# Kernel optimization log

Measured on AMD Instinct MI355X. Metric: run time of the kernel, lower is better.

The kernel has to match this reference:

```python
import jax, jax.numpy as jnp
import numpy as np

L, H, C, V, B, T, Q = 6, 8, 512, 32000, 2, 4096, 256
N = C // H
LN_EPS = 1e-5
GN_EPS = 1e-5 * 64  # matches nn.GroupNorm(n_head, C, eps=1e-05*64)


def _shift(x):
    # ZeroPad2d((0,0,1,-1)): x[t] -> x[t-1], zero at t=0
    return jnp.concatenate([jnp.zeros_like(x[:, :1]), x[:, :-1]], axis=1)


def _layernorm(x, w):
    mu = x.mean(-1, keepdims=True)
    var = jnp.var(x, axis=-1, keepdims=True)
    return (x - mu) * jax.lax.rsqrt(var + LN_EPS) * w


def _time_mix(x, maa_k, maa_v, maa_r, maa_g, tdecay, tfaaaa, Wr, Wk, Wv, Wg, Wo, gn_w, gn_b):
    Bsz, Tlen, Cd = x.shape
    xx = _shift(x) - x
    xk = x + xx * maa_k
    xv = x + xx * maa_v
    xr = x + xx * maa_r
    xg = x + xx * maa_g
    r = (xr @ Wr.T).reshape(Bsz, Tlen, H, N).transpose(0, 2, 1, 3)   # B H T N
    k = (xk @ Wk.T).reshape(Bsz, Tlen, H, N).transpose(0, 2, 3, 1)   # B H N T
    v = (xv @ Wv.T).reshape(Bsz, Tlen, H, N).transpose(0, 2, 1, 3)   # B H T N
    g = jax.nn.silu(xg @ Wg.T)
    wdec = jnp.exp(-jnp.exp(tdecay))            # [H], per-head decay in (0,1)
    u = tfaaaa                                  # [H], 'first token' bonus
    ws = (wdec ** Q)[None, :, None, None]       # state decay across a chunk
    jj = jnp.arange(Q)
    wkv = (wdec[:, None] ** (Q - 1 - jj))[None, :, None, :]  # [1,H,1,Q]
    wb = (wdec[:, None] ** jj)[None, :, :, None]              # [1,H,Q,1]
    d = jj[:, None] - jj[None, :]                              # i - j
    # intra-chunk decay matrix: W[i,j] = u (i==j), wdec^(i-j-1) (i>j), 0 (i<j)
    Wmat = jnp.where(d > 0, wdec[:, None, None] ** jnp.maximum(d - 1, 0), 0.0)
    Wmat = (Wmat + u[:, None, None] * jnp.eye(Q, dtype=x.dtype))[None]  # [1,H,Q,Q]
    nc = Tlen // Q
    rc = r.reshape(Bsz, H, nc, Q, N).transpose(2, 0, 1, 3, 4)  # [nc,B,H,Q,N]
    kc = k.reshape(Bsz, H, N, nc, Q).transpose(3, 0, 1, 2, 4)  # [nc,B,H,N,Q]
    vc = v.reshape(Bsz, H, nc, Q, N).transpose(2, 0, 1, 3, 4)  # [nc,B,H,Q,N]

    def step(state, inp):
        rr, kk, vv = inp
        y = ((rr @ kk) * Wmat) @ vv + (rr @ state) * wb
        new_state = ws * state + (kk * wkv) @ vv
        return new_state, y

    state0 = jnp.zeros((Bsz, H, N, N), dtype=x.dtype)
    _, yc = jax.lax.scan(step, state0, (rc, kc, vc))
    y = yc.transpose(1, 2, 0, 3, 4).reshape(Bsz, H, Tlen, N).transpose(0, 2, 1, 3)  # B T H N
    # GroupNorm(n_head groups) == per (b,t,h) normalization over head dim N
    mu = y.mean(-1, keepdims=True)
    var = jnp.var(y, axis=-1, keepdims=True)
    y = (y - mu) * jax.lax.rsqrt(var + GN_EPS)
    y = y.reshape(Bsz, Tlen, Cd) * gn_w + gn_b
    return (y * g) @ Wo.T


def _channel_mix(x, cmaa_k, cmaa_r, Wck, Wcv, Wcr):
    xx = _shift(x) - x
    xk = x + xx * cmaa_k
    xr = x + xx * cmaa_r
    h = jnp.square(jax.nn.relu(xk @ Wck.T))
    h = h @ Wcv.T
    return jax.nn.sigmoid(xr @ Wcr.T) * h


def _forward(idx, wte, wpe, ln1_w, ln2_w, lnf_w, maa_k, maa_v, maa_r, maa_g, tdecay, tfaaaa,
             Wr, Wk, Wv, Wg, Wo, gn_w, gn_b, cmaa_k, cmaa_r, Wck, Wcv, Wcr):
    t = idx.shape[1]
    x = wte[idx] + wpe[:t]
    for l in range(L):
        x = x + _time_mix(_layernorm(x, ln1_w[l]), maa_k[l], maa_v[l], maa_r[l], maa_g[l],
                          tdecay[l], tfaaaa[l], Wr[l], Wk[l], Wv[l], Wg[l], Wo[l], gn_w[l], gn_b[l])
        x = x + _channel_mix(_layernorm(x, ln2_w[l]), cmaa_k[l], cmaa_r[l], Wck[l], Wcv[l], Wcr[l])
    x = _layernorm(x, lnf_w)
    logits = x[:, -1:, :] @ wte.T  # targets=None path: only last position
    return logits


def setup_inputs() -> dict:
    key = jax.random.key(0)
    ks = jax.random.split(key, 12)
    idx = jax.random.randint(ks[0], (B, T), 0, V)
    # structured per-layer init tensors (exact formulas from __init__)
    ddd = np.arange(C, dtype=np.float32) / C
    hh = np.arange(H, dtype=np.float32) / (H - 1)
    maa_k = np.zeros((L, C), np.float32); maa_v = np.zeros((L, C), np.float32)
    maa_r = np.zeros((L, C), np.float32); maa_g = np.zeros((L, C), np.float32)
    tdecay = np.zeros((L, H), np.float32); tfaaaa = np.zeros((L, H), np.float32)
    cmaa_k = np.zeros((L, C), np.float32); cmaa_r = np.zeros((L, C), np.float32)
    for l in range(L):
        r0 = l / max(L - 1, 1)
        r1 = 1.0 - l / L
        maa_k[l] = 1.0 - ddd ** r1
        maa_v[l] = 1.0 - (ddd ** r1 + 0.3 * r0)
        maa_r[l] = 1.0 - ddd ** (0.5 * r1)
        maa_g[l] = 1.0 - ddd ** (0.5 * r1)
        tdecay[l] = -6.0 + 5.0 * hh ** (0.7 + 1.3 * r0)
        tfaaaa[l] = r0 * (1.0 - hh)
        cmaa_k[l] = 1.0 - ddd ** r1
        cmaa_r[l] = 1.0 - ddd ** r1
    s = 0.02
    return {
        'idx': idx,
        'wte': jax.random.normal(ks[1], (V, C), jnp.float32) * s,
        'wpe': jax.random.normal(ks[2], (T, C), jnp.float32) * s,
        'ln1_w': jnp.ones((L, C), jnp.float32),
        'ln2_w': jnp.ones((L, C), jnp.float32),
        'lnf_w': jnp.ones((C,), jnp.float32),
        'maa_k': jnp.asarray(maa_k), 'maa_v': jnp.asarray(maa_v),
        'maa_r': jnp.asarray(maa_r), 'maa_g': jnp.asarray(maa_g),
        'tdecay': jnp.asarray(tdecay), 'tfaaaa': jnp.asarray(tfaaaa),
        'Wr': jax.random.normal(ks[3], (L, C, C), jnp.float32) * s,
        'Wk': jax.random.normal(ks[4], (L, C, C), jnp.float32) * s,
        'Wv': jax.random.normal(ks[5], (L, C, C), jnp.float32) * s,
        'Wg': jax.random.normal(ks[6], (L, C, C), jnp.float32) * s,
        'Wo': jax.random.normal(ks[7], (L, C, C), jnp.float32) * (s / np.sqrt(2 * L)),
        'gn_w': jnp.ones((L, C), jnp.float32),
        'gn_b': jnp.zeros((L, C), jnp.float32),
        'cmaa_k': jnp.asarray(cmaa_k), 'cmaa_r': jnp.asarray(cmaa_r),
        'Wck': jax.random.normal(ks[8], (L, 3 * C, C), jnp.float32) * s,
        'Wcv': jax.random.normal(ks[9], (L, C, 3 * C), jnp.float32) * s,
        'Wcr': jax.random.normal(ks[10], (L, C, C), jnp.float32) * s,
    }


def reference(idx, wte, wpe, ln1_w, ln2_w, lnf_w, maa_k, maa_v, maa_r, maa_g, tdecay, tfaaaa,
              Wr, Wk, Wv, Wg, Wo, gn_w, gn_b, cmaa_k, cmaa_r, Wck, Wcv, Wcr):
    return _forward(idx, wte, wpe, ln1_w, ln2_w, lnf_w, maa_k, maa_v, maa_r, maa_g, tdecay,
                    tfaaaa, Wr, Wk, Wv, Wg, Wo, gn_w, gn_b, cmaa_k, cmaa_r, Wck, Wcv, Wcr)
```

## Files before the change

### kernel.cpp

```cpp
#include <hip/hip_runtime.h>

#define L_ 6
#define H_ 8
#define C_ 512
#define V_ 32000
#define B_ 2
#define T_ 4096
#define Q_ 256
#define N_ 64
#define NC_ 16
#define M_ 8192

typedef unsigned short u16;
typedef __attribute__((ext_vector_type(8))) short bf16x8;
typedef __attribute__((ext_vector_type(4))) float f32x4;

__device__ __forceinline__ float bf2f(u16 u){
  return __uint_as_float(((unsigned int)u) << 16);
}
__device__ __forceinline__ u16 f2bf(float f){
  unsigned int x = __float_as_uint(f);
  return (u16)((x + 0x7fffu + ((x >> 16) & 1u)) >> 16);
}

__device__ __forceinline__ void gl_lds16(const u16* g, u16* l){
  __builtin_amdgcn_global_load_lds((const __attribute__((address_space(1))) void*)g,
                                   (__attribute__((address_space(3))) void*)l, 16, 0, 0);
}

__global__ __launch_bounds__(256) void detect_kernel(const void* __restrict__ probe,
                                                     int* __restrict__ flag){
  __shared__ int cnt;
  if (threadIdx.x == 0) cnt = 0;
  __syncthreads();
  const u16* p = (const u16*)probe;
  int c = 0;
  for (int i = threadIdx.x; i < 2048; i += 256){
    int e = (p[i] >> 7) & 0xFF;
    if (e >= 128) c++;
  }
  atomicAdd(&cnt, c);
  __syncthreads();
  if (threadIdx.x == 0) *flag = (cnt > 32) ? 1 : 0;
}

struct CvtTab { const void* s[23]; u16* d[23]; int n[23]; };

__global__ __launch_bounds__(256) void convert_all(CvtTab t, const int* __restrict__ flag){
  const bool f32 = (*flag != 0);
  const int stride = gridDim.x * 256;
  #pragma unroll 1
  for (int i = 0; i < 23; i++){
    const int n8 = t.n[i] >> 3;
    const float4* sf = (const float4*)t.s[i];
    const uint4*  sh = (const uint4*)t.s[i];
    uint4* d = (uint4*)t.d[i];
    for (int j = blockIdx.x*256 + threadIdx.x; j < n8; j += stride){
      uint4 r;
      if (f32){
        float4 a = sf[2*j], b = sf[2*j+1];
        r.x = (unsigned)f2bf(a.x) | ((unsigned)f2bf(a.y) << 16);
        r.y = (unsigned)f2bf(a.z) | ((unsigned)f2bf(a.w) << 16);
        r.z = (unsigned)f2bf(b.x) | ((unsigned)f2bf(b.y) << 16);
        r.w = (unsigned)f2bf(b.z) | ((unsigned)f2bf(b.w) << 16);
      } else r = sh[j];
      d[j] = r;
    }
  }
}

__global__ __launch_bounds__(256) void embed_kernel(const int* __restrict__ idx,
    const u16* __restrict__ wte, const u16* __restrict__ wpe, float* __restrict__ x){
  int row = blockIdx.x;
  int t = row & (T_-1);
  int tok = idx[row];
  const u16* we = wte + (size_t)tok * C_;
  const u16* wp = wpe + (size_t)t * C_;
  float* xo = x + (size_t)row * C_;
  int c = threadIdx.x;
  xo[c]     = bf2f(we[c])     + bf2f(wp[c]);
  xo[c+256] = bf2f(we[c+256]) + bf2f(wp[c+256]);
}

__global__ __launch_bounds__(256) void ln_tmix_kernel(const float* __restrict__ x,
    const u16* __restrict__ w,
    const u16* __restrict__ mk, const u16* __restrict__ mv,
    const u16* __restrict__ mr, const u16* __restrict__ mg,
    u16* __restrict__ xk, u16* __restrict__ xv, u16* __restrict__ xr, u16* __restrict__ xg){
  int row = blockIdx.x; int t = row & (T_-1);
  size_t off = (size_t)row*C_;
  const float* cur = x + off;
  int c = threadIdx.x;
  float v0 = cur[c], v1 = cur[c+256];
  float p0 = 0.f, p1 = 0.f;
  if (t){ p0 = cur[c - C_]; p1 = cur[c+256 - C_]; }
  float s = v0+v1, ss = v0*v0+v1*v1;
  float sp = p0+p1, ssp = p0*p0+p1*p1;
  int lane = c & 63, wid = c >> 6;
  #pragma unroll
  for (int o=32;o>0;o>>=1){
    s  += __shfl_down(s,o,64);  ss  += __shfl_down(ss,o,64);
    sp += __shfl_down(sp,o,64); ssp += __shfl_down(ssp,o,64);
  }
  __shared__ float r1[4], r2[4], r3[4], r4[4];
  if (lane==0){ r1[wid]=s; r2[wid]=ss; r3[wid]=sp; r4[wid]=ssp; }
  __syncthreads();
  if (c==0){
    float a =r1[0]+r1[1]+r1[2]+r1[3], bq=r2[0]+r2[1]+r2[2]+r2[3];
    float ap=r3[0]+r3[1]+r3[2]+r3[3], bp=r4[0]+r4[1]+r4[2]+r4[3];
    float mu  = a *(1.f/C_); float var  = bq*(1.f/C_) - mu*mu;
    float mup = ap*(1.f/C_); float varp = bp*(1.f/C_) - mup*mup;
    r1[0]=mu;  r2[0]=rsqrtf(fmaxf(var ,0.f)+1e-5f);
    r3[0]=mup; r4[0]=rsqrtf(fmaxf(varp,0.f)+1e-5f);
  }
  __syncthreads();
  float mu=r1[0], inv=r2[0], mup=r3[0], invp=r4[0];
  #pragma unroll
  for (int p=0;p<2;p++){
    int cc = c + p*256;
    float wc = bf2f(w[cc]);
    float xc = ((p?v1:v0)-mu)*inv*wc;
    float xp = t ? ((p?p1:p0)-mup)*invp*wc : 0.f;
    float xx = xp - xc;
    xk[off+cc] = f2bf(xc + xx*bf2f(mk[cc]));
    xv[off+cc] = f2bf(xc + xx*bf2f(mv[cc]));
    xr[off+cc] = f2bf(xc + xx*bf2f(mr[cc]));
    xg[off+cc] = f2bf(xc + xx*bf2f(mg[cc]));
  }
}

__global__ __launch_bounds__(256) void ln_cmix_kernel(const float* __restrict__ x,
    const u16* __restrict__ w,
    const u16* __restrict__ mk, const u16* __restrict__ mr,
    u16* __restrict__ xk, u16* __restrict__ xr){
  int row = blockIdx.x; int t = row & (T_-1);
  size_t off = (size_t)row*C_;
  const float* cur = x + off;
  int c = threadIdx.x;
  float v0 = cur[c], v1 = cur[c+256];
  float p0 = 0.f, p1 = 0.f;
  if (t){ p0 = cur[c - C_]; p1 = cur[c+256 - C_]; }
  float s = v0+v1, ss = v0*v0+v1*v1;
  float sp = p0+p1, ssp = p0*p0+p1*p1;
  int lane = c & 63, wid = c >> 6;
  #pragma unroll
  for (int o=32;o>0;o>>=1){
    s  += __shfl_down(s,o,64);  ss  += __shfl_down(ss,o,64);
    sp += __shfl_down(sp,o,64); ssp += __shfl_down(ssp,o,64);
  }
  __shared__ float r1[4], r2[4], r3[4], r4[4];
  if (lane==0){ r1[wid]=s; r2[wid]=ss; r3[wid]=sp; r4[wid]=ssp; }
  __syncthreads();
  if (c==0){
    float a =r1[0]+r1[1]+r1[2]+r1[3], bq=r2[0]+r2[1]+r2[2]+r2[3];
    float ap=r3[0]+r3[1]+r3[2]+r3[3], bp=r4[0]+r4[1]+r4[2]+r4[3];
    float mu  = a *(1.f/C_); float var  = bq*(1.f/C_) - mu*mu;
    float mup = ap*(1.f/C_); float varp = bp*(1.f/C_) - mup*mup;
    r1[0]=mu;  r2[0]=rsqrtf(fmaxf(var ,0.f)+1e-5f);
    r3[0]=mup; r4[0]=rsqrtf(fmaxf(varp,0.f)+1e-5f);
  }
  __syncthreads();
  float mu=r1[0], inv=r2[0], mup=r3[0], invp=r4[0];
  #pragma unroll
  for (int p=0;p<2;p++){
    int cc = c + p*256;
    float wc = bf2f(w[cc]);
    float xc = ((p?v1:v0)-mu)*inv*wc;
    float xp = t ? ((p?p1:p0)-mup)*invp*wc : 0.f;
    float xx = xp - xc;
    xk[off+cc] = f2bf(xc + xx*bf2f(mk[cc]));
    xr[off+cc] = f2bf(xc + xx*bf2f(mr[cc]));
  }
}

__global__ __launch_bounds__(256) void lnf_last(const float* __restrict__ x,
    const u16* __restrict__ w, float* __restrict__ xf){
  int b = blockIdx.x;
  const float* xr = x + ((size_t)b*T_ + (T_-1))*C_;
  int c = threadIdx.x;
  float v0 = xr[c], v1 = xr[c+256];
  float s = v0+v1, ss = v0*v0+v1*v1;
  int lane = c & 63, wid = c >> 6;
  #pragma unroll
  for (int o=32;o>0;o>>=1){ s += __shfl_down(s,o,64); ss += __shfl_down(ss,o,64); }
  __shared__ float r1[4], r2[4];
  if (lane==0){ r1[wid]=s; r2[wid]=ss; }
  __syncthreads();
  if (c==0){
    float a=r1[0]+r1[1]+r1[2]+r1[3], bq=r2[0]+r2[1]+r2[2]+r2[3];
    float mu = a*(1.f/C_);
    float var = bq*(1.f/C_) - mu*mu;
    r1[0]=mu; r2[0]=rsqrtf(fmaxf(var,0.f)+1e-5f);
  }
  __syncthreads();
  float mu=r1[0], inv=r2[0];
  xf[b*C_+c]     = (v0-mu)*inv*bf2f(w[c]);
  xf[b*C_+c+256] = (v1-mu)*inv*bf2f(w[c+256]);
}

#define ACT_F32 0
#define ACT_RELU2_BF16 1
#define ACT_ADD_F32 2
#define ACT_BF16 3
#define ACT_CMIX 4

template<int ACT>
__device__ __forceinline__ void gemm_mfma_body(const u16* __restrict__ X, const u16* __restrict__ W,
    float* __restrict__ Yf, u16* __restrict__ Yb, const float* __restrict__ Aux,
    int Ndim, int Kdim, int bm, int bn){
  __shared__ __align__(16) u16 Al[128*64];
  __shared__ __align__(16) u16 Bl[64*64];
  const int tid = threadIdx.x;
  const int wv = tid >> 6, ln = tid & 63;
  const int m16 = ln & 15, q = ln >> 4;

  f32x4 acc[2][4];
  #pragma unroll
  for (int i=0;i<2;i++)
    #pragma unroll
    for (int j=0;j<4;j++) acc[i][j] = f32x4{0.f,0.f,0.f,0.f};

  const int r0 = wv*8 + (ln >> 3);
  const int c0 = (ln & 7)*8;
  const u16* ga = X + (size_t)(bm + r0)*Kdim + c0;
  const u16* gb = W + (size_t)(bn + r0)*Kdim + c0;
  u16* la = Al + r0*64 + c0;
  u16* lb = Bl + r0*64 + c0;

  for (int k0=0; k0<Kdim; k0+=64){
    #pragma unroll
    for (int s=0;s<4;s++)
      gl_lds16(ga + (size_t)(s*32)*Kdim + k0, la + s*2048);
    #pragma unroll
    for (int s=0;s<2;s++)
      gl_lds16(gb + (size_t)(s*32)*Kdim + k0, lb + s*2048);
    __syncthreads();
    #pragma unroll
    for (int kh=0; kh<2; kh++){
      bf16x8 af[2], bfr[4];
      #pragma unroll
      for (int i=0;i<2;i++) af[i]  = *(const bf16x8*)(Al + (wv*32 + i*16 + m16)*64 + kh*32 + q*8);
      #pragma unroll
      for (int j=0;j<4;j++) bfr[j] = *(const bf16x8*)(Bl + (j*16 + m16)*64 + kh*32 + q*8);
      #pragma unroll
      for (int i=0;i<2;i++)
        #pragma unroll
        for (int j=0;j<4;j++)
          acc[i][j] = __builtin_amdgcn_mfma_f32_16x16x32_bf16(af[i], bfr[j], acc[i][j], 0, 0, 0);
    }
    __syncthreads();
  }

  #pragma unroll
  for (int i=0;i<2;i++){
    int row = bm + wv*32 + i*16 + q*4;
    #pragma unroll
    for (int j=0;j<4;j++){
      int col = bn + j*16 + m16;
      #pragma unroll
      for (int r=0;r<4;r++){
        size_t off = (size_t)(row + r)*Ndim + col;
        float v = acc[i][j][r];
        if (ACT==ACT_F32) Yf[off] = v;
        else if (ACT==ACT_RELU2_BF16){ float rr = v>0.f ? v : 0.f; Yb[off] = f2bf(rr*rr); }
        else if (ACT==ACT_BF16) Yb[off] = f2bf(v);
        else if (ACT==ACT_CMIX){ float rr = Aux[off]; Yf[off] += v/(1.f+expf(-rr)); }
        else Yf[off] += v;
      }
    }
  }
}

template<int ACT>
__global__ __launch_bounds__(256,4) void gemm_mfma(const u16* __restrict__ X, const u16* __restrict__ W,
    float* __restrict__ Yf, u16* __restrict__ Yb, int Ndim, int Kdim){
  gemm_mfma_body<ACT>(X, W, Yf, Yb, nullptr, Ndim, Kdim, blockIdx.x*128, blockIdx.y*64);
}

__global__ __launch_bounds__(256,4) void gemm4_mfma(const u16* __restrict__ Abase,
    const u16* __restrict__ W0, const u16* __restrict__ W1,
    const u16* __restrict__ W2, const u16* __restrict__ W3,
    u16* __restrict__ Obase){
  const size_t MC = (size_t)M_*C_;
  const int z = blockIdx.z;
  const u16* X; const u16* W;
  switch (z){
    case 0:  X = Abase + 2*MC; W = W0; break;
    case 1:  X = Abase;        W = W1; break;
    case 2:  X = Abase + 1*MC; W = W2; break;
    default: X = Abase + 3*MC; W = W3; break;
  }
  gemm_mfma_body<ACT_BF16>(X, W, nullptr, Obase + (size_t)z*MC, nullptr, C_, C_,
                           blockIdx.x*128, blockIdx.y*64);
}

__global__ __launch_bounds__(256,4) void gemm_ck_cr(const u16* __restrict__ MK, const u16* __restrict__ Wck,
    u16* __restrict__ H1, const u16* __restrict__ MV, const u16* __restrict__ Wcr,
    float* __restrict__ RR){
  if (blockIdx.y < 24)
    gemm_mfma_body<ACT_RELU2_BF16>(MK, Wck, nullptr, H1, nullptr, 3*C_, C_,
                                   blockIdx.x*128, blockIdx.y*64);
  else
    gemm_mfma_body<ACT_F32>(MV, Wcr, RR, nullptr, nullptr, C_, C_,
                            blockIdx.x*128, (blockIdx.y-24)*64);
}

__global__ __launch_bounds__(256,4) void gemm_cmix(const u16* __restrict__ H1, const u16* __restrict__ Wcv,
    float* __restrict__ X, const float* __restrict__ RR){
  gemm_mfma_body<ACT_CMIX>(H1, Wcv, X, nullptr, RR, C_, 3*C_,
                           blockIdx.x*128, blockIdx.y*64);
}

__global__ __launch_bounds__(256) void vt_transpose(const u16* __restrict__ Vb, u16* __restrict__ Vt){
  __shared__ __align__(16) u16 tile[64*64];
  const int t0 = blockIdx.x*64, bh = blockIdx.y, b = bh>>3, h = bh&7;
  const int tid = threadIdx.x;
  #pragma unroll
  for (int it=0; it<2; ++it){
    int tl = it*32 + (tid>>3);
    int n0 = (tid&7)*8;
    uint4 v = *(const uint4*)(Vb + ((size_t)(b*T_ + t0 + tl))*C_ + h*N_ + n0);
    int col = n0 ^ (((tl>>3)&7)<<3);
    *(uint4*)&tile[tl*64 + col] = v;
  }
  __syncthreads();
  #pragma unroll
  for (int it=0; it<2; ++it){
    int nl = it*32 + (tid>>3);
    int t0l = (tid&7)*8;
    int swz = (tid&7)<<3;
    union {uint4 q; u16 h2[8];} pk;
    #pragma unroll
    for (int e=0;e<8;++e)
      pk.h2[e] = tile[(t0l+e)*64 + (nl ^ swz)];
    *(uint4*)(Vt + ((size_t)(bh*N_ + nl))*T_ + t0 + t0l) = pk.q;
  }
}

__global__ __launch_bounds__(256) void wkv_intra_mfma(const u16* __restrict__ Rb,
    const u16* __restrict__ Kb, const u16* __restrict__ Vt,
    const u16* __restrict__ td, const u16* __restrict__ tf, float* __restrict__ y){
  __shared__ float wpow[Q_];
  __shared__ __align__(16) u16 P[4][16][72];
  const int c = blockIdx.x >> 2, ip = blockIdx.x & 3;
  const int bh = blockIdx.y, b = bh >> 3, h = bh & 7;
  const int tid = threadIdx.x, wv = tid >> 6, ln = tid & 63;
  const int m16 = ln & 15, q = ln >> 4;
  const float wdec = expf(-expf(bf2f(td[h])));
  const float uu = bf2f(tf[h]);
  wpow[tid] = powf(wdec, (float)tid);
  __syncthreads();
  const size_t base = ((size_t)b*T_ + (size_t)c*Q_)*C_ + h*N_;
  const int iw0 = ip*64 + wv*16;
  const u16* rrow = Rb + base + (size_t)(iw0 + m16)*C_;
  bf16x8 af0 = *(const bf16x8*)(rrow + q*8);
  bf16x8 af1 = *(const bf16x8*)(rrow + 32 + q*8);
  f32x4 acc[4];
  #pragma unroll
  for (int nt=0;nt<4;++nt) acc[nt] = f32x4{0.f,0.f,0.f,0.f};
  const int irow = iw0 + q*4;
  const u16* vtb = Vt + (size_t)(bh*N_)*T_ + (size_t)c*Q_;
  for (int jt=0; jt<=ip; ++jt){
    f32x4 s[4];
    #pragma unroll
    for (int j2=0;j2<4;++j2) s[j2] = f32x4{0.f,0.f,0.f,0.f};
    #pragma unroll
    for (int j2=0;j2<4;++j2){
      const u16* kr = Kb + base + (size_t)(jt*64 + j2*16 + m16)*C_;
      bf16x8 b0 = *(const bf16x8*)(kr + q*8);
      bf16x8 b1 = *(const bf16x8*)(kr + 32 + q*8);
      s[j2] = __builtin_amdgcn_mfma_f32_16x16x32_bf16(af0, b0, s[j2], 0,0,0);
      s[j2] = __builtin_amdgcn_mfma_f32_16x16x32_bf16(af1, b1, s[j2], 0,0,0);
    }
    #pragma unroll
    for (int j2=0;j2<4;++j2){
      int jc = jt*64 + j2*16 + m16;
      #pragma unroll
      for (int r=0;r<4;++r){
        int ic = irow + r;
        float w = (jc < ic) ? wpow[ic-jc-1] : ((jc==ic) ? uu : 0.f);
        P[wv][q*4+r][j2*16+m16] = f2bf(s[j2][r]*w);
      }
    }
    __asm__ volatile("s_waitcnt lgkmcnt(0)" ::: "memory");
    #pragma unroll
    for (int kp=0;kp<2;++kp){
      bf16x8 ap = *(const bf16x8*)&P[wv][m16][kp*32 + q*8];
      #pragma unroll
      for (int nt=0;nt<4;++nt){
        bf16x8 bv = *(const bf16x8*)(vtb + (size_t)(nt*16 + m16)*T_ + jt*64 + kp*32 + q*8);
        acc[nt] = __builtin_amdgcn_mfma_f32_16x16x32_bf16(ap, bv, acc[nt], 0,0,0);
      }
    }
  }
  #pragma unroll
  for (int nt=0;nt<4;++nt)
    #pragma unroll
    for (int r=0;r<4;++r)
      y[base + (size_t)(irow + r)*C_ + nt*16 + m16] = acc[nt][r];
}

__global__ __launch_bounds__(256) void wkv_state(const u16* __restrict__ Kb, const u16* __restrict__ Vb,
    const u16* __restrict__ td, float* __restrict__ S){
  __shared__ float kst[64][68];
  __shared__ float vst[64][68];
  __shared__ float wpow[Q_];
  const int c = blockIdx.x, bh = blockIdx.y, b = bh>>3, h = bh&7;
  const int tid = threadIdx.x, tx = tid&15, ty = tid>>4;
  const float wdec = expf(-expf(bf2f(td[h])));
  wpow[tid] = powf(wdec, (float)tid);
  const size_t base = ((size_t)b*T_ + (size_t)c*Q_)*C_ + h*N_;
  float acc[4][4] = {};
  for (int jt=0;jt<4;++jt){
    __syncthreads();
    {
      const int rr = tid >> 6, cc2 = tid & 63;
      const int j0 = jt*64;
      for (int it=0; it<16; ++it){
        int j = it*4 + rr;
        kst[j][cc2] = bf2f(Kb[base + (size_t)(j0+j)*C_ + cc2]);
        vst[j][cc2] = bf2f(Vb[base + (size_t)(j0+j)*C_ + cc2]);
      }
    }
    __syncthreads();
    for (int jl=0;jl<64;++jl){
      float f = wpow[Q_-1-(jt*64+jl)];
      float kv[4], vv[4];
      #pragma unroll
      for (int mm=0;mm<4;mm++) kv[mm]=kst[jl][ty*4+mm]*f;
      #pragma unroll
      for (int nn=0;nn<4;nn++) vv[nn]=vst[jl][tx*4+nn];
      #pragma unroll
      for (int mm=0;mm<4;mm++)
        #pragma unroll
        for (int nn=0;nn<4;nn++) acc[mm][nn]+=kv[mm]*vv[nn];
    }
  }
  float* Sp = S + ((size_t)bh*NC_ + c)*(N_*N_);
  #pragma unroll
  for (int mm=0;mm<4;mm++)
    #pragma unroll
    for (int nn=0;nn<4;nn++)
      Sp[(ty*4+mm)*N_ + tx*4+nn] = acc[mm][nn];
}

__global__ __launch_bounds__(256) void wkv_prefix(float* __restrict__ S, const u16* __restrict__ td){
  const int bh = blockIdx.x, h = bh&7;
  const float wdec = expf(-expf(bf2f(td[h])));
  const float wsd = powf(wdec, (float)Q_);
  float* Sp = S + (size_t)bh*NC_*N_*N_;
  for (int e=threadIdx.x; e<N_*N_; e+=256){
    float cur = 0.f;
    for (int cc=0;cc<NC_;++cc){
      float sc = Sp[(size_t)cc*N_*N_ + e];
      Sp[(size_t)cc*N_*N_ + e] = cur;
      cur = wsd*cur + sc;
    }
  }
}

__global__ __launch_bounds__(256) void wkv_inter_gn(const u16* __restrict__ Rb, const float* __restrict__ S,
    const u16* __restrict__ td, const float* __restrict__ y,
    const u16* __restrict__ gnw, const u16* __restrict__ gnb, const u16* __restrict__ g,
    u16* __restrict__ out){
  __shared__ float st[64][65];
  __shared__ float rs[64][68];
  __shared__ float wpow[Q_];
  const int c = blockIdx.x>>2, ip = blockIdx.x&3;
  const int bh = blockIdx.y, b = bh>>3, h = bh&7;
  const int tid = threadIdx.x, tx = tid&15, ty = tid>>4;
  const float wdec = expf(-expf(bf2f(td[h])));
  wpow[tid] = powf(wdec, (float)tid);
  const float* Sp = S + ((size_t)bh*NC_ + c)*(N_*N_);
  for (int e=tid;e<N_*N_;e+=256) st[e>>6][e&63] = Sp[e];
  const size_t base = ((size_t)b*T_ + (size_t)c*Q_)*C_ + h*N_;
  const int i0 = ip*64;
  {
    const int rr = tid >> 6, cc2 = tid & 63;
    for (int it=0;it<16;++it){ int i=it*4+rr; rs[i][cc2]=bf2f(Rb[base+(size_t)(i0+i)*C_+cc2]); }
  }
  __syncthreads();
  float acc[4][4] = {};
  for (int kk=0;kk<N_;++kk){
    float rv[4], sv[4];
    #pragma unroll
    for (int ii=0;ii<4;ii++) rv[ii]=rs[ty*4+ii][kk];
    #pragma unroll
    for (int nn=0;nn<4;nn++) sv[nn]=st[kk][tx*4+nn];
    #pragma unroll
    for (int ii=0;ii<4;ii++)
      #pragma unroll
      for (int nn=0;nn<4;nn++) acc[ii][nn]+=rv[ii]*sv[nn];
  }
  #pragma unroll
  for (int ii=0;ii<4;ii++){
    int il = i0+ty*4+ii;
    size_t roff = base + (size_t)il*C_;
    float w = wpow[il];
    float val[4];
    float s=0.f, ss=0.f;
    #pragma unroll
    for (int nn=0;nn<4;nn++){
      float v = y[roff + tx*4+nn] + w*acc[ii][nn];
      val[nn]=v; s+=v; ss+=v*v;
    }
    #pragma unroll
    for (int o=8;o>0;o>>=1){ s+=__shfl_xor(s,o,64); ss+=__shfl_xor(ss,o,64); }
    float mu = s*(1.f/N_);
    float var = ss*(1.f/N_) - mu*mu;
    float inv = rsqrtf(fmaxf(var,0.f) + 6.4e-4f);
    #pragma unroll
    for (int nn=0;nn<4;nn++){
      int n = tx*4+nn, ci = h*N_+n;
      float gg = bf2f(g[roff+n]);
      float sil = gg/(1.f+expf(-gg));
      out[roff+n] = f2bf(((val[nn]-mu)*inv*bf2f(gnw[ci]) + bf2f(gnb[ci]))*sil);
    }
  }
}

__global__ __launch_bounds__(256) void logits_kernel(const float* __restrict__ xf,
    const u16* __restrict__ wte, void* __restrict__ out, const int* __restrict__ flag){
  const int wid = threadIdx.x>>6, lane = threadIdx.x&63;
  const int gw = blockIdx.x*4 + wid;
  const int b = gw / V_, v = gw - b*V_;
  const u16* wrow = wte + (size_t)v*C_;
  const float* xr = xf + b*C_;
  union {uint4 q; u16 h[8];} uu;
  uu.q = *(const uint4*)(wrow + lane*8);
  float s = 0.f;
  #pragma unroll
  for (int j=0;j<8;j++) s += bf2f(uu.h[j])*xr[lane*8+j];
  #pragma unroll
  for (int o=32;o>0;o>>=1) s += __shfl_down(s,o,64);
  if (lane==0){
    size_t o = (size_t)b*V_ + v;
    if (*flag) ((float*)out)[o] = s;
    else       ((u16*)out)[o]   = f2bf(s);
  }
}

extern "C" void kernel_launch(void* const* d_in, const int* in_sizes, int n_in,
                              void* d_out, int out_size, void* d_ws, size_t ws_size,
                              hipStream_t stream){
  (void)out_size; (void)ws_size; (void)n_in;
  const int* idx  = (const int*)d_in[0];

  char* ws = (char*)d_ws;
  const size_t MC  = (size_t)M_*C_;
  size_t o = 0;
  int* flag = (int*)(ws + o);            o += 1024;
  float* X   = (float*)(ws + o);         o += MC*4;
  float* Y   = (float*)(ws + o);         o += MC*4;
  u16* MK = (u16*)(ws + o);              o += MC*2;
  u16* MV = (u16*)(ws + o);              o += MC*2;
  u16* MR = (u16*)(ws + o);              o += MC*2;
  u16* MG = (u16*)(ws + o);              o += MC*2;
  u16* Rb = (u16*)(ws + o);              o += MC*2;
  u16* Kb = (u16*)(ws + o);              o += MC*2;
  u16* Vb = (u16*)(ws + o);              o += MC*2;
  u16* Gb = (u16*)(ws + o);              o += MC*2;
  u16* Vt = (u16*)(ws + o);              o += MC*2;
  float* XF = (float*)(ws + o);          o += 65536;
  u16* pool = (u16*)(ws + o);
  u16* YGN = MK;
  float* S  = (float*)MR;
  u16* H1 = Rb;
  float* RR = (float*)MR;

  detect_kernel<<<1,256,0,stream>>>(d_in[12], flag);
  u16* cw[24];
  CvtTab tab;
  {
    size_t poff = 0;
    for (int i=1;i<24;i++){
      cw[i] = pool + poff; poff += (size_t)in_sizes[i];
      tab.s[i-1] = d_in[i]; tab.d[i-1] = cw[i]; tab.n[i-1] = in_sizes[i];
    }
  }
  convert_all<<<2048,256,0,stream>>>(tab, flag);
  const u16* wte  = cw[1];  const u16* wpe  = cw[2];
  const u16* ln1w = cw[3];  const u16* ln2w = cw[4];  const u16* lnfw = cw[5];
  const u16* maak = cw[6];  const u16* maav = cw[7];
  const u16* maar = cw[8];  const u16* maag = cw[9];
  const u16* tdec = cw[10]; const u16* tfir = cw[11];
  const u16* Wr   = cw[12]; const u16* Wk   = cw[13]; const u16* Wv   = cw[14];
  const u16* Wg   = cw[15]; const u16* Wo   = cw[16];
  const u16* gnw  = cw[17]; const u16* gnb  = cw[18];
  const u16* cmk  = cw[19]; const u16* cmr  = cw[20];
  const u16* Wck  = cw[21]; const u16* Wcv  = cw[22]; const u16* Wcr  = cw[23];

  embed_kernel<<<M_,256,0,stream>>>(idx,wte,wpe,X);
  dim3 gsq(M_/128, C_/64);
  dim3 g4 (M_/128, C_/64, 4);
  dim3 gckcr(M_/128, 32);
  for (int l=0;l<L_;++l){
    ln_tmix_kernel<<<M_,256,0,stream>>>(X, ln1w+l*C_, maak+l*C_, maav+l*C_, maar+l*C_,
                                        maag+l*C_, MK,MV,MR,MG);
    gemm4_mfma<<<g4,256,0,stream>>>(MK, Wr+(size_t)l*C_*C_, Wk+(size_t)l*C_*C_,
                                    Wv+(size_t)l*C_*C_, Wg+(size_t)l*C_*C_, Rb);
    vt_transpose<<<dim3(T_/64, B_*H_),256,0,stream>>>(Vb, Vt);
    wkv_intra_mfma<<<dim3(NC_*4, B_*H_),256,0,stream>>>(Rb,Kb,Vt, tdec+l*H_, tfir+l*H_, Y);
    wkv_state<<<dim3(NC_,   B_*H_),256,0,stream>>>(Kb,Vb, tdec+l*H_, S);
    wkv_prefix<<<B_*H_,256,0,stream>>>(S, tdec+l*H_);
    wkv_inter_gn<<<dim3(NC_*4, B_*H_),256,0,stream>>>(Rb, S, tdec+l*H_, Y,
                                                      gnw+l*C_, gnb+l*C_, Gb, YGN);
    gemm_mfma<ACT_ADD_F32><<<gsq,256,0,stream>>>(YGN, Wo+(size_t)l*C_*C_, X, nullptr, C_, C_);
    ln_cmix_kernel<<<M_,256,0,stream>>>(X, ln2w+l*C_, cmk+l*C_, cmr+l*C_, MK, MV);
    gemm_ck_cr<<<gckcr,256,0,stream>>>(MK, Wck+(size_t)l*3*C_*C_, H1,
                                       MV, Wcr+(size_t)l*C_*C_, RR);
    gemm_cmix<<<gsq,256,0,stream>>>(H1, Wcv+(size_t)l*C_*3*C_, X, RR);
  }
  lnf_last<<<B_,256,0,stream>>>(X, lnfw, XF);
  logits_kernel<<<(B_*V_)/4,256,0,stream>>>(XF, wte, d_out, flag);
}
```

Before: 1.653 ms.

## Fuse K/V transposes into projection GEMM epilogue and use MFMA for chunk state

The K and V projection GEMM epilogues now write transposed copies directly: V as Vt, and K as a decay-prescaled Kt. This removes the separate vt_transpose kernel and the V row-major buffer. The per-chunk state kernel is rewritten to use bf16 MFMA on Kt/Vt in place of the scalar fp32 LDS outer-product loop. The GroupNorm epilogue is vectorised and the weight conversion becomes a single flat loop over all tensors. The trade-offs are scattered 8-byte transposed stores from the GEMM, powf work in the epilogue, and bf16 rounding of the decay-scaled K that feeds the state.

```diff
diff --git a/kernel.cpp b/kernel.cpp
--- a/kernel.cpp
+++ b/kernel.cpp
@@ -44,28 +44,31 @@
   if (threadIdx.x == 0) *flag = (cnt > 32) ? 1 : 0;
 }
 
-struct CvtTab { const void* s[23]; u16* d[23]; int n[23]; };
-
-__global__ __launch_bounds__(256) void convert_all(CvtTab t, const int* __restrict__ flag){
+struct CvtTab { const void* s[23]; int off8[24]; };
+
+__global__ __launch_bounds__(256) void convert_all(CvtTab t, u16* __restrict__ pool,
+                                                   const int* __restrict__ flag){
   const bool f32 = (*flag != 0);
+  const int total = t.off8[23];
+  uint4* dp = (uint4*)pool;
   const int stride = gridDim.x * 256;
-  #pragma unroll 1
-  for (int i = 0; i < 23; i++){
-    const int n8 = t.n[i] >> 3;
-    const float4* sf = (const float4*)t.s[i];
-    const uint4*  sh = (const uint4*)t.s[i];
-    uint4* d = (uint4*)t.d[i];
-    for (int j = blockIdx.x*256 + threadIdx.x; j < n8; j += stride){
-      uint4 r;
-      if (f32){
-        float4 a = sf[2*j], b = sf[2*j+1];
-        r.x = (unsigned)f2bf(a.x) | ((unsigned)f2bf(a.y) << 16);
-        r.y = (unsigned)f2bf(a.z) | ((unsigned)f2bf(a.w) << 16);
-        r.z = (unsigned)f2bf(b.x) | ((unsigned)f2bf(b.y) << 16);
-        r.w = (unsigned)f2bf(b.z) | ((unsigned)f2bf(b.w) << 16);
-      } else r = sh[j];
-      d[j] = r;
-    }
+  for (int j = blockIdx.x*256 + threadIdx.x; j < total; j += stride){
+    int i = 0;
+    #pragma unroll
+    for (int k = 1; k < 23; k++) if (j >= t.off8[k]) i = k;
+    const int loc = j - t.off8[i];
+    uint4 r;
+    if (f32){
+      const float4* sf = (const float4*)t.s[i];
+      float4 a = sf[2*loc], b = sf[2*loc+1];
+      r.x = (unsigned)f2bf(a.x) | ((unsigned)f2bf(a.y) << 16);
+      r.y = (unsigned)f2bf(a.z) | ((unsigned)f2bf(a.w) << 16);
+      r.z = (unsigned)f2bf(b.x) | ((unsigned)f2bf(b.y) << 16);
+      r.w = (unsigned)f2bf(b.z) | ((unsigned)f2bf(b.w) << 16);
+    } else {
+      r = ((const uint4*)t.s[i])[loc];
+    }
+    dp[j] = r;
   }
 }
 
@@ -203,10 +206,13 @@
 #define ACT_ADD_F32 2
 #define ACT_BF16 3
 #define ACT_CMIX 4
+#define ACT_KT 5
+#define ACT_VT 6
 
 template<int ACT>
 __device__ __forceinline__ void gemm_mfma_body(const u16* __restrict__ X, const u16* __restrict__ W,
     float* __restrict__ Yf, u16* __restrict__ Yb, const float* __restrict__ Aux,
+    u16* __restrict__ Yt, const u16* __restrict__ td,
     int Ndim, int Kdim, int bm, int bn){
   __shared__ __align__(16) u16 Al[128*64];
   __shared__ __align__(16) u16 Bl[64*64];
@@ -251,6 +257,40 @@
     __syncthreads();
   }
 
+  if (ACT==ACT_KT || ACT==ACT_VT){
+    float wdec_s = 0.f;
+    if (ACT==ACT_KT) wdec_s = expf(-expf(bf2f(td[bn>>6])));
+    #pragma unroll
+    for (int i=0;i<2;i++){
+      int row = bm + wv*32 + i*16 + q*4;
+      int bb = row >> 12;
+      int tt = row & (T_-1);
+      int tloc = row & (Q_-1);
+      float wsc[4];
+      if (ACT==ACT_KT){
+        #pragma unroll
+        for (int r=0;r<4;r++) wsc[r] = powf(wdec_s, (float)(Q_-1-tloc-r));
+      }
+      #pragma unroll
+      for (int j=0;j<4;j++){
+        int col = bn + j*16 + m16;
+        int hh = col >> 6, n = col & 63;
+        union { ushort4 v; u16 e[4]; } pk;
+        #pragma unroll
+        for (int r=0;r<4;r++){
+          float v = acc[i][j][r];
+          if (ACT==ACT_KT){
+            Yb[(size_t)(row+r)*Ndim + col] = f2bf(v);
+            pk.e[r] = f2bf(v * wsc[r]);
+          } else {
+            pk.e[r] = f2bf(v);
+          }
+        }
+        *(ushort4*)(Yt + ((size_t)((bb*8+hh)*64 + n))*T_ + tt) = pk.v;
+      }
+    }
+    return;
+  }
   #pragma unroll
   for (int i=0;i<2;i++){
     int row = bm + wv*32 + i*16 + q*4;
@@ -274,67 +314,44 @@
 template<int ACT>
 __global__ __launch_bounds__(256,4) void gemm_mfma(const u16* __restrict__ X, const u16* __restrict__ W,
     float* __restrict__ Yf, u16* __restrict__ Yb, int Ndim, int Kdim){
-  gemm_mfma_body<ACT>(X, W, Yf, Yb, nullptr, Ndim, Kdim, blockIdx.x*128, blockIdx.y*64);
+  gemm_mfma_body<ACT>(X, W, Yf, Yb, nullptr, nullptr, nullptr, Ndim, Kdim,
+                      blockIdx.x*128, blockIdx.y*64);
 }
 
 __global__ __launch_bounds__(256,4) void gemm4_mfma(const u16* __restrict__ Abase,
     const u16* __restrict__ W0, const u16* __restrict__ W1,
     const u16* __restrict__ W2, const u16* __restrict__ W3,
-    u16* __restrict__ Obase){
+    u16* __restrict__ Rb, u16* __restrict__ Kb, u16* __restrict__ Kt,
+    u16* __restrict__ Vt, u16* __restrict__ Gb, const u16* __restrict__ td){
   const size_t MC = (size_t)M_*C_;
-  const int z = blockIdx.z;
-  const u16* X; const u16* W;
-  switch (z){
-    case 0:  X = Abase + 2*MC; W = W0; break;
-    case 1:  X = Abase;        W = W1; break;
-    case 2:  X = Abase + 1*MC; W = W2; break;
-    default: X = Abase + 3*MC; W = W3; break;
-  }
-  gemm_mfma_body<ACT_BF16>(X, W, nullptr, Obase + (size_t)z*MC, nullptr, C_, C_,
-                           blockIdx.x*128, blockIdx.y*64);
+  const int bm = blockIdx.x*128, bn = blockIdx.y*64;
+  switch (blockIdx.z){
+    case 0:  gemm_mfma_body<ACT_BF16>(Abase + 2*MC, W0, nullptr, Rb, nullptr, nullptr, nullptr,
+                                      C_, C_, bm, bn); break;
+    case 1:  gemm_mfma_body<ACT_KT>(Abase, W1, nullptr, Kb, nullptr, Kt, td,
+                                    C_, C_, bm, bn); break;
+    case 2:  gemm_mfma_body<ACT_VT>(Abase + 1*MC, W2, nullptr, nullptr, nullptr, Vt, nullptr,
+                                    C_, C_, bm, bn); break;
+    default: gemm_mfma_body<ACT_BF16>(Abase + 3*MC, W3, nullptr, Gb, nullptr, nullptr, nullptr,
+                                      C_, C_, bm, bn); break;
+  }
 }
 
 __global__ __launch_bounds__(256,4) void gemm_ck_cr(const u16* __restrict__ MK, const u16* __restrict__ Wck,
     u16* __restrict__ H1, const u16* __restrict__ MV, const u16* __restrict__ Wcr,
     float* __restrict__ RR){
   if (blockIdx.y < 24)
-    gemm_mfma_body<ACT_RELU2_BF16>(MK, Wck, nullptr, H1, nullptr, 3*C_, C_,
+    gemm_mfma_body<ACT_RELU2_BF16>(MK, Wck, nullptr, H1, nullptr, nullptr, nullptr, 3*C_, C_,
                                    blockIdx.x*128, blockIdx.y*64);
   else
-    gemm_mfma_body<ACT_F32>(MV, Wcr, RR, nullptr, nullptr, C_, C_,
+    gemm_mfma_body<ACT_F32>(MV, Wcr, RR, nullptr, nullptr, nullptr, nullptr, C_, C_,
                             blockIdx.x*128, (blockIdx.y-24)*64);
 }
 
 __global__ __launch_bounds__(256,4) void gemm_cmix(const u16* __restrict__ H1, const u16* __restrict__ Wcv,
     float* __restrict__ X, const float* __restrict__ RR){
-  gemm_mfma_body<ACT_CMIX>(H1, Wcv, X, nullptr, RR, C_, 3*C_,
+  gemm_mfma_body<ACT_CMIX>(H1, Wcv, X, nullptr, RR, nullptr, nullptr, C_, 3*C_,
                            blockIdx.x*128, blockIdx.y*64);
-}
-
-__global__ __launch_bounds__(256) void vt_transpose(const u16* __restrict__ Vb, u16* __restrict__ Vt){
-  __shared__ __align__(16) u16 tile[64*64];
-  const int t0 = blockIdx.x*64, bh = blockIdx.y, b = bh>>3, h = bh&7;
-  const int tid = threadIdx.x;
-  #pragma unroll
-  for (int it=0; it<2; ++it){
-    int tl = it*32 + (tid>>3);
-    int n0 = (tid&7)*8;
-    uint4 v = *(const uint4*)(Vb + ((size_t)(b*T_ + t0 + tl))*C_ + h*N_ + n0);
-    int col = n0 ^ (((tl>>3)&7)<<3);
-    *(uint4*)&tile[tl*64 + col] = v;
-  }
-  __syncthreads();
-  #pragma unroll
-  for (int it=0; it<2; ++it){
-    int nl = it*32 + (tid>>3);
-    int t0l = (tid&7)*8;
-    int swz = (tid&7)<<3;
-    union {uint4 q; u16 h2[8];} pk;
-    #pragma unroll
-    for (int e=0;e<8;++e)
-      pk.h2[e] = tile[(t0l+e)*64 + (nl ^ swz)];
-    *(uint4*)(Vt + ((size_t)(bh*N_ + nl))*T_ + t0 + t0l) = pk.q;
-  }
 }
 
 __global__ __launch_bounds__(256) void wkv_intra_mfma(const u16* __restrict__ Rb,
@@ -400,48 +417,31 @@
       y[base + (size_t)(irow + r)*C_ + nt*16 + m16] = acc[nt][r];
 }
 
-__global__ __launch_bounds__(256) void wkv_state(const u16* __restrict__ Kb, const u16* __restrict__ Vb,
-    const u16* __restrict__ td, float* __restrict__ S){
-  __shared__ float kst[64][68];
-  __shared__ float vst[64][68];
-  __shared__ float wpow[Q_];
-  const int c = blockIdx.x, bh = blockIdx.y, b = bh>>3, h = bh&7;
-  const int tid = threadIdx.x, tx = tid&15, ty = tid>>4;
-  const float wdec = expf(-expf(bf2f(td[h])));
-  wpow[tid] = powf(wdec, (float)tid);
-  const size_t base = ((size_t)b*T_ + (size_t)c*Q_)*C_ + h*N_;
-  float acc[4][4] = {};
-  for (int jt=0;jt<4;++jt){
-    __syncthreads();
-    {
-      const int rr = tid >> 6, cc2 = tid & 63;
-      const int j0 = jt*64;
-      for (int it=0; it<16; ++it){
-        int j = it*4 + rr;
-        kst[j][cc2] = bf2f(Kb[base + (size_t)(j0+j)*C_ + cc2]);
-        vst[j][cc2] = bf2f(Vb[base + (size_t)(j0+j)*C_ + cc2]);
-      }
-    }
-    __syncthreads();
-    for (int jl=0;jl<64;++jl){
-      float f = wpow[Q_-1-(jt*64+jl)];
-      float kv[4], vv[4];
-      #pragma unroll
-      for (int mm=0;mm<4;mm++) kv[mm]=kst[jl][ty*4+mm]*f;
-      #pragma unroll
-      for (int nn=0;nn<4;nn++) vv[nn]=vst[jl][tx*4+nn];
-      #pragma unroll
-      for (int mm=0;mm<4;mm++)
-        #pragma unroll
-        for (int nn=0;nn<4;nn++) acc[mm][nn]+=kv[mm]*vv[nn];
+__global__ __launch_bounds__(256) void wkv_state_mfma(const u16* __restrict__ Kt,
+    const u16* __restrict__ Vt, float* __restrict__ S){
+  const int c = blockIdx.x, bh = blockIdx.y;
+  const int tid = threadIdx.x, wv = tid >> 6, ln = tid & 63;
+  const int m16 = ln & 15, q = ln >> 4;
+  const u16* ka = Kt + (size_t)(bh*N_ + wv*16 + m16)*T_ + c*Q_;
+  const u16* vb = Vt + (size_t)(bh*N_ + m16)*T_ + c*Q_;
+  f32x4 acc[4];
+  #pragma unroll
+  for (int nt=0;nt<4;++nt) acc[nt] = f32x4{0.f,0.f,0.f,0.f};
+  #pragma unroll
+  for (int ks=0; ks<8; ++ks){
+    bf16x8 af = *(const bf16x8*)(ka + ks*32 + q*8);
+    #pragma unroll
+    for (int nt=0;nt<4;++nt){
+      bf16x8 bv = *(const bf16x8*)(vb + (size_t)(nt*16)*T_ + ks*32 + q*8);
+      acc[nt] = __builtin_amdgcn_mfma_f32_16x16x32_bf16(af, bv, acc[nt], 0,0,0);
     }
   }
   float* Sp = S + ((size_t)bh*NC_ + c)*(N_*N_);
   #pragma unroll
-  for (int mm=0;mm<4;mm++)
-    #pragma unroll
-    for (int nn=0;nn<4;nn++)
-      Sp[(ty*4+mm)*N_ + tx*4+nn] = acc[mm][nn];
+  for (int nt=0;nt<4;++nt)
+    #pragma unroll
+    for (int r=0;r<4;++r)
+      Sp[(wv*16 + q*4 + r)*N_ + nt*16 + m16] = acc[nt][r];
 }
 
 __global__ __launch_bounds__(256) void wkv_prefix(float* __restrict__ S, const u16* __restrict__ td){
@@ -497,11 +497,12 @@
     int il = i0+ty*4+ii;
     size_t roff = base + (size_t)il*C_;
     float w = wpow[il];
-    float val[4];
+    float4 yv = *(const float4*)(y + roff + tx*4);
+    float val[4] = {yv.x, yv.y, yv.z, yv.w};
     float s=0.f, ss=0.f;
     #pragma unroll
     for (int nn=0;nn<4;nn++){
-      float v = y[roff + tx*4+nn] + w*acc[ii][nn];
+      float v = val[nn] + w*acc[ii][nn];
       val[nn]=v; s+=v; ss+=v*v;
     }
     #pragma unroll
@@ -509,13 +510,16 @@
     float mu = s*(1.f/N_);
     float var = ss*(1.f/N_) - mu*mu;
     float inv = rsqrtf(fmaxf(var,0.f) + 6.4e-4f);
+    union { ushort4 v; u16 e[4]; } gv, ov;
+    gv.v = *(const ushort4*)(g + roff + tx*4);
     #pragma unroll
     for (int nn=0;nn<4;nn++){
-      int n = tx*4+nn, ci = h*N_+n;
-      float gg = bf2f(g[roff+n]);
+      int ci = h*N_ + tx*4 + nn;
+      float gg = bf2f(gv.e[nn]);
       float sil = gg/(1.f+expf(-gg));
-      out[roff+n] = f2bf(((val[nn]-mu)*inv*bf2f(gnw[ci]) + bf2f(gnb[ci]))*sil);
-    }
+      ov.e[nn] = f2bf(((val[nn]-mu)*inv*bf2f(gnw[ci]) + bf2f(gnb[ci]))*sil);
+    }
+    *(ushort4*)(out + roff + tx*4) = ov.v;
   }
 }
 
@@ -558,7 +562,7 @@
   u16* MG = (u16*)(ws + o);              o += MC*2;
   u16* Rb = (u16*)(ws + o);              o += MC*2;
   u16* Kb = (u16*)(ws + o);              o += MC*2;
-  u16* Vb = (u16*)(ws + o);              o += MC*2;
+  u16* Kt = (u16*)(ws + o);              o += MC*2;
   u16* Gb = (u16*)(ws + o);              o += MC*2;
   u16* Vt = (u16*)(ws + o);              o += MC*2;
   float* XF = (float*)(ws + o);          o += 65536;
@@ -573,12 +577,16 @@
   CvtTab tab;
   {
     size_t poff = 0;
+    int acc8 = 0;
+    tab.off8[0] = 0;
     for (int i=1;i<24;i++){
       cw[i] = pool + poff; poff += (size_t)in_sizes[i];
-      tab.s[i-1] = d_in[i]; tab.d[i-1] = cw[i]; tab.n[i-1] = in_sizes[i];
-    }
-  }
-  convert_all<<<2048,256,0,stream>>>(tab, flag);
+      tab.s[i-1] = d_in[i];
+      acc8 += in_sizes[i] >> 3;
+      tab.off8[i] = acc8;
+    }
+  }
+  convert_all<<<2048,256,0,stream>>>(tab, pool, flag);
   const u16* wte  = cw[1];  const u16* wpe  = cw[2];
   const u16* ln1w = cw[3];  const u16* ln2w = cw[4];  const u16* lnfw = cw[5];
   const u16* maak = cw[6];  const u16* maav = cw[7];
@@ -598,10 +606,10 @@
     ln_tmix_kernel<<<M_,256,0,stream>>>(X, ln1w+l*C_, maak+l*C_, maav+l*C_, maar+l*C_,
                                         maag+l*C_, MK,MV,MR,MG);
     gemm4_mfma<<<g4,256,0,stream>>>(MK, Wr+(size_t)l*C_*C_, Wk+(size_t)l*C_*C_,
-                                    Wv+(size_t)l*C_*C_, Wg+(size_t)l*C_*C_, Rb);
-    vt_transpose<<<dim3(T_/64, B_*H_),256,0,stream>>>(Vb, Vt);
+                                    Wv+(size_t)l*C_*C_, Wg+(size_t)l*C_*C_,
+                                    Rb, Kb, Kt, Vt, Gb, tdec+l*H_);
     wkv_intra_mfma<<<dim3(NC_*4, B_*H_),256,0,stream>>>(Rb,Kb,Vt, tdec+l*H_, tfir+l*H_, Y);
-    wkv_state<<<dim3(NC_,   B_*H_),256,0,stream>>>(Kb,Vb, tdec+l*H_, S);
+    wkv_state_mfma<<<dim3(NC_, B_*H_),256,0,stream>>>(Kt, Vt, S);
     wkv_prefix<<<B_*H_,256,0,stream>>>(S, tdec+l*H_);
     wkv_inter_gn<<<dim3(NC_*4, B_*H_),256,0,stream>>>(Rb, S, tdec+l*H_, Y,
                                                       gnw+l*C_, gnb+l*C_, Gb, YGN);
```

After: 1.667 ms. No clear change (+0.8%).
